# Kernel optimization log

Measured on AMD Instinct MI355X. Metric: run time of the kernel, lower is better.

## Reference

```python
import jax, jax.numpy as jnp
import numpy as np

B, N, D, H = 128, 197, 384, 1536  # batch, patches+CLS, embed_dim, hidden_dim


def _layer_norm(x, g, b, eps=1e-5):
    m = jnp.mean(x, axis=-1, keepdims=True)
    v = jnp.mean(jnp.square(x - m), axis=-1, keepdims=True)
    return (x - m) * jax.lax.rsqrt(v + eps) * g + b


def setup_inputs() -> dict:
    key = jax.random.key(0)
    ks = jax.random.split(key, 8)
    x = jax.random.normal(ks[0], (B, N, D), dtype=jnp.float32)
    # quantum circuit surrogates: orthogonal-style square matrices
    V = jax.random.normal(ks[1], (D, D), dtype=jnp.float32) / np.sqrt(D)
    W = jax.random.normal(ks[2], (D, D), dtype=jnp.float32) / np.sqrt(D)
    ln1_g = jnp.ones((D,), jnp.float32); ln1_b = jnp.zeros((D,), jnp.float32)
    ln2_g = jnp.ones((D,), jnp.float32); ln2_b = jnp.zeros((D,), jnp.float32)
    W1 = jax.random.normal(ks[3], (D, H), dtype=jnp.float32) / np.sqrt(D)
    b1 = jnp.zeros((H,), jnp.float32)
    W2 = jax.random.normal(ks[4], (H, D), dtype=jnp.float32) / np.sqrt(H)
    b2 = jnp.zeros((D,), jnp.float32)
    return {"x": x, "ln1_g": ln1_g, "ln1_b": ln1_b, "V": V, "W": W,
            "ln2_g": ln2_g, "ln2_b": ln2_b, "W1": W1, "b1": b1, "W2": W2, "b2": b2}


def reference(x, ln1_g, ln1_b, V, W, ln2_g, ln2_b, W1, b1, W2, b2):
    inp = _layer_norm(x, ln1_g, ln1_b)
    # normalization across the patch axis (dim=1), exactly as in the torch code
    inp = inp / jnp.sqrt(jnp.sum(jnp.square(inp) + 1e-4, axis=1, keepdims=True) + 1e-8)
    # Vx circuit: unary-basis probabilities |(V x_i)_d|^2 -> vx[b, d, i]
    vx = jnp.square(jnp.einsum('de,bne->bdn', V, inp))            # [B, D, N]
    # xWx circuit: (x_i^T W x_j)^2 -> xwx[b, i, j]
    y = jnp.einsum('bnd,de->bne', inp, W)                         # [B, N, D]
    xwx = jnp.square(jnp.einsum('bne,bme->bnm', y, inp))          # [B, N, N]
    vx = jnp.sqrt(vx + 1e-8)
    xwx = jnp.sqrt(xwx + 1e-8)
    attn = jax.nn.softmax(xwx, axis=-1)                           # [B, N, N]
    t = jnp.einsum('bnm,bdm->bnd', attn, vx)                      # attn @ vx^T
    x = x + t
    h = _layer_norm(x, ln2_g, ln2_b)
    h = jax.nn.gelu(h @ W1 + b1) @ W2 + b2                        # dropout=0 (eval)
    return x + h
```

## Files before the change

### kernel.cpp

```cpp
#include <hip/hip_runtime.h>
#include <math.h>

typedef unsigned short u16;
typedef unsigned int u32;
typedef __bf16 bfv8 __attribute__((ext_vector_type(8)));
typedef float f32x4 __attribute__((ext_vector_type(4)));

#define BB 128
#define NN 197
#define DD 384
#define HH 1536
#define BN (BB*NN)
#define NP 224

__device__ __forceinline__ u16 f2bf(float x){ u32 u; __builtin_memcpy(&u,&x,4); u = (u + 0x7fffu + ((u>>16)&1u))>>16; return (u16)u; }

__device__ __forceinline__ float fast_gelu(float z){
  float t2 = 1.5957691216f*z*(1.f + 0.044715f*z*z);
  return z * __builtin_amdgcn_rcpf(1.f + __expf(-t2));
}

__device__ __forceinline__ void gload16(const void* g, void* s){
  __builtin_amdgcn_global_load_lds(
      (const __attribute__((address_space(1))) void*)g,
      (__attribute__((address_space(3))) void*)s, 16, 0, 0);
}

__global__ __launch_bounds__(256) void ln1_stats(const float* __restrict__ x,
    float* __restrict__ mu, float* __restrict__ rv){
  int row = blockIdx.x*4 + (threadIdx.x>>6);
  int lane = threadIdx.x & 63;
  const float* xr = x + (long)row*DD;
  float s=0.f, ss=0.f;
  #pragma unroll
  for (int j=0;j<DD/64;j++){ float v = xr[lane + j*64]; s+=v; ss+=v*v; }
  #pragma unroll
  for (int m=32;m;m>>=1){ s += __shfl_xor(s,m); ss += __shfl_xor(ss,m); }
  if (lane==0){
    float mn = s*(1.f/DD);
    float var = ss*(1.f/DD) - mn*mn;
    mu[row]=mn; rv[row]=1.f/sqrtf(var+1e-5f);
  }
}

__global__ __launch_bounds__(256) void colnorm(const float* __restrict__ x,
    const float* __restrict__ mu, const float* __restrict__ rv,
    const float* __restrict__ g, const float* __restrict__ bt,
    float* __restrict__ scale){
  int i = blockIdx.x*256 + threadIdx.x;
  int b = i/DD, d = i - b*DD;
  const float* xp = x + (long)b*NN*DD + d;
  float gd = g[d], bd = bt[d];
  float s = 0.f;
  for (int n=0;n<NN;n++){
    float v = (xp[(long)n*DD] - mu[b*NN+n]) * rv[b*NN+n] * gd + bd;
    s += v*v;
  }
  scale[i] = 1.f/sqrtf(s + 197.f*1e-4f + 1e-8f);
}

__global__ __launch_bounds__(256) void ln_apply(const float* __restrict__ x,
    const float* __restrict__ mu, const float* __restrict__ rv,
    const float* __restrict__ g, const float* __restrict__ bt,
    const float* __restrict__ scale, u16* __restrict__ inpn){
  long i = (long)blockIdx.x*256 + threadIdx.x;
  int d = (int)(i % DD);
  long row = i / DD;
  int b = (int)(row / NN);
  float v = (x[i]-mu[row])*rv[row]*g[d]+bt[d];
  inpn[i] = f2bf(v * scale[b*DD+d]);
}

__global__ __launch_bounds__(256) void prep_weights(const float* __restrict__ V, const float* __restrict__ W,
    const float* __restrict__ W1, const float* __restrict__ W2,
    u16* __restrict__ Vb, u16* __restrict__ Wt, u16* __restrict__ W1t, u16* __restrict__ W2t){
  int i = blockIdx.x*256 + threadIdx.x;
  if (i < DD*DD){
    Vb[i] = f2bf(V[i]);
    int r = i/DD, c = i - r*DD;
    Wt[c*DD + r] = f2bf(W[i]);
  }
  {
    int r = i/HH, c = i - r*HH;
    W1t[(long)c*DD + r] = f2bf(W1[i]);
    int r2 = i/DD, c2 = i - r2*DD;
    W2t[(long)c2*HH + r2] = f2bf(W2[i]);
  }
}

__global__ __launch_bounds__(256) void softmax_rows(const float* __restrict__ S, u16* __restrict__ attn){
  int row = blockIdx.x*4 + (threadIdx.x>>6);
  int lane = threadIdx.x & 63;
  const float* sr = S + (long)row*NP;
  float v[4]; float mx = -1e30f;
  #pragma unroll
  for (int j=0;j<4;j++){ int c = lane + j*64; v[j] = (c<NN)? sr[c] : -1e30f; mx = fmaxf(mx, v[j]); }
  #pragma unroll
  for (int m=32;m;m>>=1) mx = fmaxf(mx, __shfl_xor(mx,m));
  float sm = 0.f;
  #pragma unroll
  for (int j=0;j<4;j++){ v[j] = __expf(v[j]-mx); sm += v[j]; }
  #pragma unroll
  for (int m=32;m;m>>=1) sm += __shfl_xor(sm,m);
  float inv = __builtin_amdgcn_rcpf(sm);
  u16* ar = attn + (long)row*NP;
  #pragma unroll
  for (int j=0;j<4;j++){ int c = lane + j*64; if (c<NP) ar[c] = f2bf(v[j]*inv); }
}

__global__ __launch_bounds__(256) void ln2_fused(const float* __restrict__ x2,
    const float* __restrict__ g, const float* __restrict__ bt, u16* __restrict__ h){
  int row = blockIdx.x*4 + (threadIdx.x>>6);
  int lane = threadIdx.x & 63;
  const float* xr = x2 + (long)row*DD;
  float v[6]; float s=0.f, ss=0.f;
  #pragma unroll
  for (int j=0;j<6;j++){ v[j]=xr[lane+j*64]; s+=v[j]; ss+=v[j]*v[j]; }
  #pragma unroll
  for (int m=32;m;m>>=1){ s+=__shfl_xor(s,m); ss+=__shfl_xor(ss,m); }
  float mn = s*(1.f/DD);
  float rvv = 1.f/sqrtf(ss*(1.f/DD)-mn*mn+1e-5f);
  u16* hr = h + (long)row*DD;
  #pragma unroll
  for (int j=0;j<6;j++){ int d = lane+j*64; hr[d] = f2bf((v[j]-mn)*rvv*g[d]+bt[d]); }
}

struct EpiUt { u16* ut;
  __device__ void operator()(int, int r0, int c, const f32x4* col) const {
    #pragma unroll
    for (int m=0;m<4;m++)
      #pragma unroll
      for (int i=0;i<4;i++){
        int r = r0 + m*16 + i;
        int b = r/NN, p = r - b*NN;
        float v = col[m][i];
        ut[((long)b*DD + c)*NP + p] = f2bf(sqrtf(v*v + 1e-8f));
      }
  }};
struct EpiY { u16* y;
  __device__ void operator()(int, int r0, int c, const f32x4* col) const {
    u16* yp = y + (long)r0*DD + c;
    #pragma unroll
    for (int m=0;m<4;m++)
      #pragma unroll
      for (int i=0;i<4;i++)
        yp[(long)(m*16+i)*DD] = f2bf(col[m][i]);
  }};
struct EpiS { float* s;
  __device__ void operator()(int b, int r0, int c, const f32x4* col) const {
    float* sp = s + ((long)b*NN + r0)*NP + c;
    #pragma unroll
    for (int m=0;m<4;m++)
      #pragma unroll
      for (int i=0;i<4;i++){
        int r = r0 + m*16 + i;
        float v = col[m][i];
        if (r < NN) sp[(long)(m*16+i)*NP] = sqrtf(v*v + 1e-8f);
      }
  }};
struct EpiX2 { float* x2; const float* x;
  __device__ void operator()(int b, int r0, int c, const f32x4* col) const {
    long base = ((long)b*NN + r0)*DD + c;
    #pragma unroll
    for (int m=0;m<4;m++)
      #pragma unroll
      for (int i=0;i<4;i++){
        int r = r0 + m*16 + i;
        if (r < NN){ long idx = base + (long)(m*16+i)*DD; x2[idx] = x[idx] + col[m][i]; }
      }
  }};
struct EpiGelu { u16* g; const float* b1;
  __device__ void operator()(int, int r0, int c, const f32x4* col) const {
    float bb = b1[c];
    u16* gp = g + (long)r0*HH + c;
    #pragma unroll
    for (int m=0;m<4;m++)
      #pragma unroll
      for (int i=0;i<4;i++)
        gp[(long)(m*16+i)*HH] = f2bf(fast_gelu(col[m][i] + bb));
  }};
struct EpiOut { float* o; const float* x2; const float* b2;
  __device__ void operator()(int, int r0, int c, const f32x4* col) const {
    float bb = b2[c];
    long base = (long)r0*DD + c;
    #pragma unroll
    for (int m=0;m<4;m++)
      #pragma unroll
      for (int i=0;i<4;i++){
        long idx = base + (long)(m*16+i)*DD;
        o[idx] = x2[idx] + col[m][i] + bb;
      }
  }};

template<class Epi>
__global__ __launch_bounds__(256) void gemm_nt(const u16* __restrict__ A, const u16* __restrict__ B,
    int M, int N, int K, int lda, int ldb, long sA, long sB, int NT, Epi epi)
{
  __shared__ __align__(16) u16 As[128*32];
  __shared__ __align__(16) u16 Bs[128*32];
  int wg;
  { int flat = blockIdx.x, nwg = gridDim.x;
    int xcd = flat & 7, local = flat >> 3;
    int q = nwg >> 3, r = nwg & 7;
    wg = (xcd < r ? xcd*(q+1) : r*(q+1) + (xcd-r)*q) + local; }
  const int bm = wg / NT, bn = wg - bm*NT;
  const int bat = blockIdx.y;
  const u16* Ab = A + (long)bat*sA;
  const u16* Bb = B + (long)bat*sB;
  const int t = threadIdx.x, lane = t&63, wid = t>>6, wr = wid>>1, wc = wid&1;
  const int row0 = bm*128, col0 = bn*128;

  long aoff[2], boff[2]; int soff[2];
  #pragma unroll
  for (int i=0;i<2;i++){
    int ob = (i*256+t)*16;
    int r = ob>>6;
    int ke = (ob&63)>>1;
    int ra = row0+r; if (ra>M-1) ra=M-1;
    int rb = col0+r; if (rb>N-1) rb=N-1;
    aoff[i] = (long)ra*lda + ke;
    boff[i] = (long)rb*ldb + ke;
    soff[i] = ob;
  }

  f32x4 acc[4][4] = {};
  const int kg = (lane>>4)*8, rl = lane&15;

  for (int k0=0; k0<K; k0+=32){
    #pragma unroll
    for (int i=0;i<2;i++){
      gload16(Ab + aoff[i] + k0, (char*)As + soff[i]);
      gload16(Bb + boff[i] + k0, (char*)Bs + soff[i]);
    }
    __syncthreads();
    bfv8 af[4], bfr[4];
    #pragma unroll
    for (int m=0;m<4;m++) af[m]  = *(const bfv8*)&As[(wr*64 + m*16 + rl)*32 + kg];
    #pragma unroll
    for (int n=0;n<4;n++) bfr[n] = *(const bfv8*)&Bs[(wc*64 + n*16 + rl)*32 + kg];
    #pragma unroll
    for (int m=0;m<4;m++)
      #pragma unroll
      for (int n=0;n<4;n++)
        acc[m][n] = __builtin_amdgcn_mfma_f32_16x16x32_bf16(af[m], bfr[n], acc[m][n], 0,0,0);
    __syncthreads();
  }

  const int rbase = row0 + wr*64 + (lane>>4)*4;
  const int cbase = col0 + wc*64 + rl;
  #pragma unroll
  for (int n=0;n<4;n++){
    int c = cbase + n*16;
    if (c < N){
      f32x4 colv[4] = {acc[0][n], acc[1][n], acc[2][n], acc[3][n]};
      epi(bat, rbase, c, colv);
    }
  }
}

extern "C" void kernel_launch(void* const* d_in, const int* in_sizes, int n_in,
                              void* d_out, int out_size, void* d_ws, size_t ws_size,
                              hipStream_t stream){
  const float* x     = (const float*)d_in[0];
  const float* g1    = (const float*)d_in[1];
  const float* b1n   = (const float*)d_in[2];
  const float* V     = (const float*)d_in[3];
  const float* W     = (const float*)d_in[4];
  const float* g2    = (const float*)d_in[5];
  const float* b2n   = (const float*)d_in[6];
  const float* W1    = (const float*)d_in[7];
  const float* bias1 = (const float*)d_in[8];
  const float* W2    = (const float*)d_in[9];
  const float* bias2 = (const float*)d_in[10];
  float* out = (float*)d_out;

  char* ws = (char*)d_ws;
  size_t off = 0;
  auto take = [&](size_t bytes)->char*{ char* p = ws + off; off += (bytes + 255) & ~(size_t)255; return p; };

  float* mu    = (float*)take((size_t)BN*4);
  float* rv    = (float*)take((size_t)BN*4);
  float* scale = (float*)take((size_t)BB*DD*4);
  char* aliasBase = ws + off;
  u16*  inpn = (u16*) take((size_t)BN*DD*2);
  u16*  Ut   = (u16*) take((size_t)BB*DD*NP*2);
  u16*  Yb   = (u16*) take((size_t)BN*DD*2);
  float* S   = (float*)take((size_t)BN*NP*4);
  u16*  attn = (u16*) take((size_t)BN*NP*2);
  float* x2  = (float*)take((size_t)BN*DD*4);
  u16*  h    = (u16*) take((size_t)BN*DD*2);
  u16*  Vb   = (u16*) take((size_t)DD*DD*2);
  u16*  Wt   = (u16*) take((size_t)DD*DD*2);
  u16*  W1t  = (u16*) take((size_t)DD*HH*2);
  u16*  W2t  = (u16*) take((size_t)DD*HH*2);
  u16*  G    = (u16*)aliasBase;

  prep_weights<<<DD*HH/256, 256, 0, stream>>>(V, W, W1, W2, Vb, Wt, W1t, W2t);
  ln1_stats  <<<BN/4,       256, 0, stream>>>(x, mu, rv);
  colnorm    <<<BB*DD/256,  256, 0, stream>>>(x, mu, rv, g1, b1n, scale);
  ln_apply   <<<BN*DD/256,  256, 0, stream>>>(x, mu, rv, g1, b1n, scale, inpn);
  (void)hipMemsetAsync(Ut, 0, (size_t)BB*DD*NP*2, stream);

  { dim3 grid(197*3, 1);
    gemm_nt<EpiUt><<<grid,256,0,stream>>>(inpn, Vb, BN, DD, DD, DD, DD, 0, 0, 3, EpiUt{Ut}); }
  { dim3 grid(197*3, 1);
    gemm_nt<EpiY><<<grid,256,0,stream>>>(inpn, Wt, BN, DD, DD, DD, DD, 0, 0, 3, EpiY{Yb}); }
  { dim3 grid(4, BB);
    gemm_nt<EpiS><<<grid,256,0,stream>>>(Yb, inpn, NN, NN, DD, DD, DD,
                                         (long)NN*DD, (long)NN*DD, 2, EpiS{S}); }
  softmax_rows<<<BN/4, 256, 0, stream>>>(S, attn);
  { dim3 grid(6, BB);
    gemm_nt<EpiX2><<<grid,256,0,stream>>>(attn, Ut, NN, DD, NP, NP, NP,
                                          (long)NN*NP, (long)DD*NP, 3, EpiX2{x2, x}); }
  ln2_fused<<<BN/4, 256, 0, stream>>>(x2, g2, b2n, h);
  { dim3 grid(197*12, 1);
    gemm_nt<EpiGelu><<<grid,256,0,stream>>>(h, W1t, BN, HH, DD, DD, DD, 0, 0, 12, EpiGelu{G, bias1}); }
  { dim3 grid(197*3, 1);
    gemm_nt<EpiOut><<<grid,256,0,stream>>>(G, W2t, BN, DD, HH, HH, HH, 0, 0, 3, EpiOut{out, x2, bias2}); }
}
```

Measured before the change: 432.2 us.

## Double-buffer GEMM LDS tiles and use 64-row tiles for smaller GEMMs

The GEMM kernel is templated on the M tile size and gets two LDS buffers, so the next K-slice is prefetched while the current one feeds the MFMAs. Most GEMMs, including the attention and projection ones, switch to 64-row tiles to launch more workgroups and cut padding waste on the 197-row batches. The FFN up-projection keeps 128-row tiles. The trade-off is more LDS per block and lower per-block arithmetic intensity.

Measured after the change: 433.3 us. About the same (+0.3%).

```diff
diff --git a/kernel.cpp b/kernel.cpp
--- a/kernel.cpp
+++ b/kernel.cpp
@@ -126,9 +126,8 @@
 }
 
 struct EpiUt { u16* ut;
-  __device__ void operator()(int, int r0, int c, const f32x4* col) const {
-    #pragma unroll
-    for (int m=0;m<4;m++)
+  __device__ void operator()(int, int r0, int c, const f32x4* col, int mf) const {
+    for (int m=0;m<mf;m++)
       #pragma unroll
       for (int i=0;i<4;i++){
         int r = r0 + m*16 + i;
@@ -138,19 +137,17 @@
       }
   }};
 struct EpiY { u16* y;
-  __device__ void operator()(int, int r0, int c, const f32x4* col) const {
+  __device__ void operator()(int, int r0, int c, const f32x4* col, int mf) const {
     u16* yp = y + (long)r0*DD + c;
-    #pragma unroll
-    for (int m=0;m<4;m++)
+    for (int m=0;m<mf;m++)
       #pragma unroll
       for (int i=0;i<4;i++)
         yp[(long)(m*16+i)*DD] = f2bf(col[m][i]);
   }};
 struct EpiS { float* s;
-  __device__ void operator()(int b, int r0, int c, const f32x4* col) const {
+  __device__ void operator()(int b, int r0, int c, const f32x4* col, int mf) const {
     float* sp = s + ((long)b*NN + r0)*NP + c;
-    #pragma unroll
-    for (int m=0;m<4;m++)
+    for (int m=0;m<mf;m++)
       #pragma unroll
       for (int i=0;i<4;i++){
         int r = r0 + m*16 + i;
@@ -159,10 +156,9 @@
       }
   }};
 struct EpiX2 { float* x2; const float* x;
-  __device__ void operator()(int b, int r0, int c, const f32x4* col) const {
+  __device__ void operator()(int b, int r0, int c, const f32x4* col, int mf) const {
     long base = ((long)b*NN + r0)*DD + c;
-    #pragma unroll
-    for (int m=0;m<4;m++)
+    for (int m=0;m<mf;m++)
       #pragma unroll
       for (int i=0;i<4;i++){
         int r = r0 + m*16 + i;
@@ -170,21 +166,19 @@
       }
   }};
 struct EpiGelu { u16* g; const float* b1;
-  __device__ void operator()(int, int r0, int c, const f32x4* col) const {
+  __device__ void operator()(int, int r0, int c, const f32x4* col, int mf) const {
     float bb = b1[c];
     u16* gp = g + (long)r0*HH + c;
-    #pragma unroll
-    for (int m=0;m<4;m++)
+    for (int m=0;m<mf;m++)
       #pragma unroll
       for (int i=0;i<4;i++)
         gp[(long)(m*16+i)*HH] = f2bf(fast_gelu(col[m][i] + bb));
   }};
 struct EpiOut { float* o; const float* x2; const float* b2;
-  __device__ void operator()(int, int r0, int c, const f32x4* col) const {
+  __device__ void operator()(int, int r0, int c, const f32x4* col, int mf) const {
     float bb = b2[c];
     long base = (long)r0*DD + c;
-    #pragma unroll
-    for (int m=0;m<4;m++)
+    for (int m=0;m<mf;m++)
       #pragma unroll
       for (int i=0;i<4;i++){
         long idx = base + (long)(m*16+i)*DD;
@@ -192,12 +186,14 @@
       }
   }};
 
-template<class Epi>
+template<int BM, class Epi>
 __global__ __launch_bounds__(256) void gemm_nt(const u16* __restrict__ A, const u16* __restrict__ B,
     int M, int N, int K, int lda, int ldb, long sA, long sB, int NT, Epi epi)
 {
-  __shared__ __align__(16) u16 As[128*32];
-  __shared__ __align__(16) u16 Bs[128*32];
+  constexpr int MF = BM/32;
+  constexpr int ALOADS = BM/64;
+  __shared__ __align__(16) u16 As[2][BM*32];
+  __shared__ __align__(16) u16 Bs[2][128*32];
   int wg;
   { int flat = blockIdx.x, nwg = gridDim.x;
     int xcd = flat & 7, local = flat >> 3;
@@ -208,52 +204,65 @@
   const u16* Ab = A + (long)bat*sA;
   const u16* Bb = B + (long)bat*sB;
   const int t = threadIdx.x, lane = t&63, wid = t>>6, wr = wid>>1, wc = wid&1;
-  const int row0 = bm*128, col0 = bn*128;
-
-  long aoff[2], boff[2]; int soff[2];
+  const int row0 = bm*BM, col0 = bn*128;
+
+  long aoff[ALOADS]; int asoff[ALOADS];
+  #pragma unroll
+  for (int i=0;i<ALOADS;i++){
+    int ob = (i*256+t)*16;
+    int r = ob>>6, ke = (ob&63)>>1;
+    int ra = row0+r; if (ra>M-1) ra=M-1;
+    aoff[i] = (long)ra*lda + ke; asoff[i] = ob;
+  }
+  long boff[2]; int bsoff[2];
   #pragma unroll
   for (int i=0;i<2;i++){
     int ob = (i*256+t)*16;
-    int r = ob>>6;
-    int ke = (ob&63)>>1;
-    int ra = row0+r; if (ra>M-1) ra=M-1;
+    int r = ob>>6, ke = (ob&63)>>1;
     int rb = col0+r; if (rb>N-1) rb=N-1;
-    aoff[i] = (long)ra*lda + ke;
-    boff[i] = (long)rb*ldb + ke;
-    soff[i] = ob;
-  }
-
-  f32x4 acc[4][4] = {};
+    boff[i] = (long)rb*ldb + ke; bsoff[i] = ob;
+  }
+
+  auto stage = [&](int buf, int k0){
+    #pragma unroll
+    for (int i=0;i<ALOADS;i++) gload16(Ab + aoff[i] + k0, (char*)As[buf] + asoff[i]);
+    #pragma unroll
+    for (int i=0;i<2;i++)      gload16(Bb + boff[i] + k0, (char*)Bs[buf] + bsoff[i]);
+  };
+
+  f32x4 acc[MF][4] = {};
   const int kg = (lane>>4)*8, rl = lane&15;
-
-  for (int k0=0; k0<K; k0+=32){
-    #pragma unroll
-    for (int i=0;i<2;i++){
-      gload16(Ab + aoff[i] + k0, (char*)As + soff[i]);
-      gload16(Bb + boff[i] + k0, (char*)Bs + soff[i]);
-    }
-    __syncthreads();
-    bfv8 af[4], bfr[4];
-    #pragma unroll
-    for (int m=0;m<4;m++) af[m]  = *(const bfv8*)&As[(wr*64 + m*16 + rl)*32 + kg];
-    #pragma unroll
-    for (int n=0;n<4;n++) bfr[n] = *(const bfv8*)&Bs[(wc*64 + n*16 + rl)*32 + kg];
-    #pragma unroll
-    for (int m=0;m<4;m++)
+  const int ntile = K/32;
+
+  stage(0, 0);
+  __syncthreads();
+  int buf = 0;
+  for (int tt=0; tt<ntile; ++tt){
+    if (tt+1 < ntile) stage(buf^1, (tt+1)*32);
+    bfv8 af[MF], bfr[4];
+    #pragma unroll
+    for (int m=0;m<MF;m++) af[m]  = *(const bfv8*)&As[buf][(wr*(BM/2) + m*16 + rl)*32 + kg];
+    #pragma unroll
+    for (int n=0;n<4;n++)  bfr[n] = *(const bfv8*)&Bs[buf][(wc*64 + n*16 + rl)*32 + kg];
+    #pragma unroll
+    for (int m=0;m<MF;m++)
       #pragma unroll
       for (int n=0;n<4;n++)
         acc[m][n] = __builtin_amdgcn_mfma_f32_16x16x32_bf16(af[m], bfr[n], acc[m][n], 0,0,0);
     __syncthreads();
-  }
-
-  const int rbase = row0 + wr*64 + (lane>>4)*4;
+    buf ^= 1;
+  }
+
+  const int rbase = row0 + wr*(BM/2) + (lane>>4)*4;
   const int cbase = col0 + wc*64 + rl;
   #pragma unroll
   for (int n=0;n<4;n++){
     int c = cbase + n*16;
     if (c < N){
-      f32x4 colv[4] = {acc[0][n], acc[1][n], acc[2][n], acc[3][n]};
-      epi(bat, rbase, c, colv);
+      f32x4 colv[MF];
+      #pragma unroll
+      for (int m=0;m<MF;m++) colv[m] = acc[m][n];
+      epi(bat, rbase, c, colv, MF);
     }
   }
 }
@@ -301,20 +310,20 @@
   ln_apply   <<<BN*DD/256,  256, 0, stream>>>(x, mu, rv, g1, b1n, scale, inpn);
   (void)hipMemsetAsync(Ut, 0, (size_t)BB*DD*NP*2, stream);
 
-  { dim3 grid(197*3, 1);
-    gemm_nt<EpiUt><<<grid,256,0,stream>>>(inpn, Vb, BN, DD, DD, DD, DD, 0, 0, 3, EpiUt{Ut}); }
-  { dim3 grid(197*3, 1);
-    gemm_nt<EpiY><<<grid,256,0,stream>>>(inpn, Wt, BN, DD, DD, DD, DD, 0, 0, 3, EpiY{Yb}); }
-  { dim3 grid(4, BB);
-    gemm_nt<EpiS><<<grid,256,0,stream>>>(Yb, inpn, NN, NN, DD, DD, DD,
+  { dim3 grid(394*3, 1);
+    gemm_nt<64,EpiUt><<<grid,256,0,stream>>>(inpn, Vb, BN, DD, DD, DD, DD, 0, 0, 3, EpiUt{Ut}); }
+  { dim3 grid(394*3, 1);
+    gemm_nt<64,EpiY><<<grid,256,0,stream>>>(inpn, Wt, BN, DD, DD, DD, DD, 0, 0, 3, EpiY{Yb}); }
+  { dim3 grid(4*2, BB);
+    gemm_nt<64,EpiS><<<grid,256,0,stream>>>(Yb, inpn, NN, NN, DD, DD, DD,
                                          (long)NN*DD, (long)NN*DD, 2, EpiS{S}); }
   softmax_rows<<<BN/4, 256, 0, stream>>>(S, attn);
-  { dim3 grid(6, BB);
-    gemm_nt<EpiX2><<<grid,256,0,stream>>>(attn, Ut, NN, DD, NP, NP, NP,
+  { dim3 grid(4*3, BB);
+    gemm_nt<64,EpiX2><<<grid,256,0,stream>>>(attn, Ut, NN, DD, NP, NP, NP,
                                           (long)NN*NP, (long)DD*NP, 3, EpiX2{x2, x}); }
   ln2_fused<<<BN/4, 256, 0, stream>>>(x2, g2, b2n, h);
   { dim3 grid(197*12, 1);
-    gemm_nt<EpiGelu><<<grid,256,0,stream>>>(h, W1t, BN, HH, DD, DD, DD, 0, 0, 12, EpiGelu{G, bias1}); }
-  { dim3 grid(197*3, 1);
-    gemm_nt<EpiOut><<<grid,256,0,stream>>>(G, W2t, BN, DD, HH, HH, HH, 0, 0, 3, EpiOut{out, x2, bias2}); }
-}
+    gemm_nt<128,EpiGelu><<<grid,256,0,stream>>>(h, W1t, BN, HH, DD, DD, DD, 0, 0, 12, EpiGelu{G, bias1}); }
+  { dim3 grid(394*3, 1);
+    gemm_nt<64,EpiOut><<<grid,256,0,stream>>>(G, W2t, BN, DD, HH, HH, HH, 0, 0, 3, EpiOut{out, x2, bias2}); }
+}
```
